# Performance work log

Measured on AMD Instinct MI355X. Metric: run time of the kernel, lower is better.

## Reference

```python
import jax, jax.numpy as jnp
import numpy as np

N = 98304        # total nodes (= 16384 graphs * act_dim 6)
E = 1572864      # edges (avg degree 16)
C = 64           # in_channels
H = 32           # hidden_size
ACT = 6          # act_dim


def setup_inputs() -> dict:
    key = jax.random.key(0)
    ks = jax.random.split(key, 11)
    s = lambda fan: 1.0 / np.sqrt(fan)
    return {
        "state": jax.random.normal(ks[0], (N, C), jnp.float32),
        "edge_index": jax.random.randint(ks[1], (2, E), 0, N, dtype=jnp.int64),
        "conv_W": jax.random.normal(ks[2], (C, C), jnp.float32) * s(C),
        "conv_b": jax.random.normal(ks[3], (C,), jnp.float32) * 0.01,
        "W1": jax.random.normal(ks[4], (C, H), jnp.float32) * s(C),
        "b1": jax.random.normal(ks[5], (H,), jnp.float32) * 0.01,
        "W2": jax.random.normal(ks[6], (H, H), jnp.float32) * s(H),
        "b2": jax.random.normal(ks[7], (H,), jnp.float32) * 0.01,
        "W3": jax.random.normal(ks[8], (H, 1), jnp.float32) * s(H),
        "b3": jax.random.normal(ks[9], (1,), jnp.float32) * 0.01,
    }


def gcn_conv(x, edge_index, W, b):
    # PyG GCNConv: add self-loops, symmetric normalization D^-1/2 (A+I) D^-1/2 (X W) + b
    loops = jnp.arange(N, dtype=edge_index.dtype)
    src = jnp.concatenate([edge_index[0], loops])  # [E+N]
    dst = jnp.concatenate([edge_index[1], loops])  # [E+N]
    deg = jax.ops.segment_sum(jnp.ones(E + N, x.dtype), dst, num_segments=N)
    dinv = jax.lax.rsqrt(deg)                      # deg >= 1 due to self-loops
    norm = dinv[src] * dinv[dst]                   # [E+N]
    h = x @ W                                      # [N, C]
    msg = h[src] * norm[:, None]                   # gather + scale
    return jax.ops.segment_sum(msg, dst, num_segments=N) + b


def reference(state, edge_index, conv_W, conv_b, W1, b1, W2, b2, W3, b3):
    out = jax.nn.relu(gcn_conv(state, edge_index, conv_W, conv_b))
    x = out + state                                # residual
    x = x.reshape(-1, ACT, C)                      # [num_graphs, act_dim, C]
    x = jax.nn.relu(x @ W1 + b1)
    x = jax.nn.relu(x @ W2 + b2)
    x = jax.nn.softplus(x @ W3 + b3)
    concentration = x.squeeze(-1) + 1e-20          # [num_graphs, act_dim]
    return concentration
```

## Files before the change

### kernel.cpp

```cpp
#include <hip/hip_runtime.h>
#include <math.h>

#define Nn 98304
#define Ee 1572864
#define Cc 64
#define Hh 32
#define TT 128
#define NT (Nn / TT)
#define HB 256
#define EPB (Ee / HB)
#define CAPT 2560
#define GN 64


__device__ __forceinline__ int detect64(const void* ei) {
    const unsigned int* u = (const unsigned int*)ei;
    int is64 = 1;
    #pragma unroll
    for (int i = 0; i < 16; ++i) is64 &= (u[2 * i + 1] == 0u);
    return is64;
}

__device__ __forceinline__ int load_idx(const void* ei, long e, int is64) {
    if (is64) return (int)((const long long*)ei)[e];
    return ((const int*)ei)[e];
}

__device__ __forceinline__ unsigned short f2bf(float x) {
    union { float f; unsigned int u; } v; v.f = x;
    unsigned int r = v.u + 0x7FFFu + ((v.u >> 16) & 1u);
    return (unsigned short)(r >> 16);
}
__device__ __forceinline__ float bf2f(unsigned short h) {
    union { unsigned int u; float f; } v; v.u = ((unsigned int)h) << 16;
    return v.f;
}

__device__ __forceinline__ void acc_u4(float a[8], uint4 u) {
    union { unsigned int i; float f; } w;
    w.i = u.x << 16;         a[0] += w.f;
    w.i = u.x & 0xFFFF0000u; a[1] += w.f;
    w.i = u.y << 16;         a[2] += w.f;
    w.i = u.y & 0xFFFF0000u; a[3] += w.f;
    w.i = u.z << 16;         a[4] += w.f;
    w.i = u.z & 0xFFFF0000u; a[5] += w.f;
    w.i = u.w << 16;         a[6] += w.f;
    w.i = u.w & 0xFFFF0000u; a[7] += w.f;
}
__device__ __forceinline__ void set_u4(float a[8], uint4 u) {
    union { unsigned int i; float f; } w;
    w.i = u.x << 16;         a[0] = w.f;
    w.i = u.x & 0xFFFF0000u; a[1] = w.f;
    w.i = u.y << 16;         a[2] = w.f;
    w.i = u.y & 0xFFFF0000u; a[3] = w.f;
    w.i = u.z << 16;         a[4] = w.f;
    w.i = u.z & 0xFFFF0000u; a[5] = w.f;
    w.i = u.w << 16;         a[6] = w.f;
    w.i = u.w & 0xFFFF0000u; a[7] = w.f;
}

__global__ __launch_bounds__(1024) void k_bucket(const void* __restrict__ ei,
                                                 unsigned int* __restrict__ aux,
                                                 unsigned int* __restrict__ ebuf) {
    __shared__ unsigned int hl[NT];
    __shared__ unsigned int off[NT];
    int t = threadIdx.x, b = blockIdx.x;
    if (t < NT) hl[t] = 0;
    __syncthreads();
    int is64 = detect64(ei);
    long e0 = (long)b * EPB;
    #pragma unroll
    for (int i = 0; i < EPB / 1024; ++i) {
        int d = load_idx(ei, (long)Ee + e0 + i * 1024 + t, is64);
        atomicAdd(&hl[d >> 7], 1u);
    }
    __syncthreads();
    if (t < NT) off[t] = hl[t];
    __syncthreads();
    for (int s = 1; s < NT; s <<= 1) {
        unsigned int v = (t < NT && t >= s) ? off[t - s] : 0u;
        __syncthreads();
        if (t < NT) off[t] += v;
        __syncthreads();
    }
    if (t < NT) {
        unsigned int ex = off[t] - hl[t];
        aux[(long)b * NT + t] = ex | (hl[t] << 16);
        off[t] = ex;
    }
    __syncthreads();
    #pragma unroll
    for (int i = 0; i < EPB / 1024; ++i) {
        long e = e0 + i * 1024 + t;
        int s = load_idx(ei, e, is64);
        int d = load_idx(ei, (long)Ee + e, is64);
        unsigned int pos = atomicAdd(&off[d >> 7], 1u);
        ebuf[(long)b * EPB + pos] = (unsigned int)s | ((unsigned int)(d & (TT - 1)) << 17);
    }
}

__global__ __launch_bounds__(256) void k_nodecnt(const unsigned int* __restrict__ aux,
                                                 const unsigned int* __restrict__ ebuf,
                                                 unsigned int* __restrict__ rowOff,
                                                 unsigned int* __restrict__ rowEnd,
                                                 float* __restrict__ dinv,
                                                 unsigned int* __restrict__ srcs) {
    __shared__ unsigned int stage[CAPT];
    __shared__ unsigned int rb[HB];
    __shared__ unsigned int cnt[TT];
    __shared__ unsigned int sc[TT];
    __shared__ unsigned int cur[TT];
    int t = threadIdx.x, tile = blockIdx.x;
    unsigned int av = aux[(long)t * NT + tile];
    unsigned int roff = av & 0xFFFFu, rcnt = av >> 16;
    rb[t] = rcnt;
    __syncthreads();
    for (int s = 1; s < HB; s <<= 1) {
        unsigned int v = (t >= s) ? rb[t - s] : 0u;
        __syncthreads();
        rb[t] += v;
        __syncthreads();
    }
    unsigned int mybase = rb[t] - rcnt;
    for (unsigned int i = 0; i < rcnt; ++i)
        stage[mybase + i] = ebuf[(long)t * EPB + roff + i];
    if (t < TT) cnt[t] = 0;
    __syncthreads();
    int total = (int)rb[HB - 1];
    for (int i = t; i < total; i += 256)
        atomicAdd(&cnt[stage[i] >> 17], 1u);
    __syncthreads();
    if (t < TT) sc[t] = cnt[t];
    __syncthreads();
    #pragma unroll
    for (int off = 1; off < TT; off <<= 1) {
        unsigned int v = (t >= off && t < TT) ? sc[t - off] : 0u;
        __syncthreads();
        if (t < TT) sc[t] += v;
        __syncthreads();
    }
    if (t < TT) {
        unsigned int start = (unsigned int)(tile * CAPT) + sc[t] - cnt[t];
        rowOff[(long)tile * TT + t] = start;
        rowEnd[(long)tile * TT + t] = start + cnt[t];
        cur[t] = start;
        dinv[(long)tile * TT + t] = rsqrtf((float)(cnt[t] + 1));
    }
    __syncthreads();
    for (int i = t; i < total; i += 256) {
        unsigned int u = stage[i];
        unsigned int pos = atomicAdd(&cur[u >> 17], 1u);
        srcs[pos] = u & 0x1FFFFu;
    }
}

__global__ __launch_bounds__(256) void k_gemm(const float* __restrict__ state,
                                              const float* __restrict__ W,
                                              const float* __restrict__ dinv,
                                              unsigned short* __restrict__ gb) {
    __shared__ float Wl[64 * 64];
    __shared__ float Al[64 * 68];
    int t = threadIdx.x;
    long n0 = (long)blockIdx.x * 64;

    const float4* W4 = (const float4*)W;
    float4* Wl4 = (float4*)Wl;
    #pragma unroll
    for (int i = 0; i < 4; ++i) Wl4[i * 256 + t] = W4[i * 256 + t];

    const float4* S4 = (const float4*)(state) + n0 * 16;
    #pragma unroll
    for (int i = 0; i < 4; ++i) {
        int f4 = t + i * 256;
        int r = f4 >> 4, k0 = (f4 & 15) * 4;
        *(float4*)(Al + r * 68 + k0) = S4[f4];
    }
    __syncthreads();

    int r0 = (t >> 4) * 4;
    int c0 = (t & 15) * 4;
    float acc[4][4] = {{0.f}};
    #pragma unroll
    for (int kk = 0; kk < 64; kk += 4) {
        float4 a4[4], w4[4];
        #pragma unroll
        for (int i = 0; i < 4; ++i) a4[i] = *(const float4*)(Al + (r0 + i) * 68 + kk);
        #pragma unroll
        for (int j = 0; j < 4; ++j) w4[j] = *(const float4*)(Wl + (kk + j) * 64 + c0);
        const float* aa = (const float*)a4;
        const float* ww = (const float*)w4;
        #pragma unroll
        for (int i = 0; i < 4; ++i)
            #pragma unroll
            for (int j = 0; j < 4; ++j) {
                float av = aa[i * 4 + j];
                #pragma unroll
                for (int c = 0; c < 4; ++c)
                    acc[i][c] = fmaf(av, ww[j * 4 + c], acc[i][c]);
            }
    }
    #pragma unroll
    for (int i = 0; i < 4; ++i) {
        long n = n0 + r0 + i;
        float dv = dinv[n];
        ushort4 o;
        o.x = f2bf(acc[i][0] * dv); o.y = f2bf(acc[i][1] * dv);
        o.z = f2bf(acc[i][2] * dv); o.w = f2bf(acc[i][3] * dv);
        *(ushort4*)(gb + n * 64 + c0) = o;
    }
}

__global__ __launch_bounds__(512) void k_gf(const unsigned int* __restrict__ rowOff,
                                            const unsigned int* __restrict__ rowEnd,
                                            const unsigned int* __restrict__ srcs,
                                            const unsigned short* __restrict__ gb,
                                            const float* __restrict__ dinv,
                                            const float* __restrict__ state,
                                            const float* __restrict__ conv_b,
                                            const float* __restrict__ W1,
                                            const float* __restrict__ b1,
                                            const float* __restrict__ W2,
                                            const float* __restrict__ b2,
                                            const float* __restrict__ W3,
                                            const float* __restrict__ b3,
                                            float* __restrict__ out) {
    __shared__ float sa[GN * 68];
    __shared__ float hs[GN * 34];
    __shared__ float sW1[Cc * Hh];
    __shared__ float sW2[Hh * Hh];
    __shared__ float sW3[Hh], sb1[Hh], sb2[Hh], scb[Cc];
    __shared__ float sb3;
    int t = threadIdx.x;
    int wave = t >> 6, lane = t & 63;
    long n0 = (long)blockIdx.x * GN;

    for (int i = t; i < Cc * Hh; i += 512) sW1[i] = W1[i];
    for (int i = t; i < Hh * Hh; i += 512) sW2[i] = W2[i];
    if (t < Hh) { sW3[t] = W3[t]; sb1[t] = b1[t]; sb2[t] = b2[t]; }
    if (t >= 64 && t < 128) scb[t - 64] = conv_b[t - 64];
    if (t == 511) sb3 = b3[0];

    {
        int g = lane >> 3;
        int cs = lane & 7;
        int j = wave * 8 + g;
        long n = n0 + j;
        int ptr = (int)rowOff[n];
        int end = (int)rowEnd[n];
        float dv = dinv[n];
        const uint4* gb4 = (const uint4*)gb;

        float a[8];
        set_u4(a, gb4[n * 8 + cs]);

        int cnt = end - ptr;
        while (cnt >= 4) {
            int s0 = (int)srcs[ptr];
            int s1 = (int)srcs[ptr + 1];
            int s2 = (int)srcs[ptr + 2];
            int s3 = (int)srcs[ptr + 3];
            uint4 u0 = gb4[(long)s0 * 8 + cs];
            uint4 u1 = gb4[(long)s1 * 8 + cs];
            uint4 u2 = gb4[(long)s2 * 8 + cs];
            uint4 u3 = gb4[(long)s3 * 8 + cs];
            acc_u4(a, u0); acc_u4(a, u1); acc_u4(a, u2); acc_u4(a, u3);
            ptr += 4; cnt -= 4;
        }
        while (cnt > 0) {
            int s0 = (int)srcs[ptr];
            uint4 u0 = gb4[(long)s0 * 8 + cs];
            acc_u4(a, u0);
            ++ptr; --cnt;
        }

        float* r = sa + j * 68 + cs * 8;
        float4 lo, hi;
        lo.x = a[0] * dv; lo.y = a[1] * dv; lo.z = a[2] * dv; lo.w = a[3] * dv;
        hi.x = a[4] * dv; hi.y = a[5] * dv; hi.z = a[6] * dv; hi.w = a[7] * dv;
        *(float4*)r = lo;
        *(float4*)(r + 4) = hi;
    }
    __syncthreads();

    {
        int j = t >> 3, o = t & 7;
        long n = n0 + j;
        int k0 = o * 8;
        const float4* sp4 = (const float4*)(state + n * 64 + k0);
        float4 s0 = sp4[0], s1 = sp4[1];
        float* r = sa + j * 68 + k0;
        r[0] = fmaxf(r[0] + scb[k0 + 0], 0.f) + s0.x;
        r[1] = fmaxf(r[1] + scb[k0 + 1], 0.f) + s0.y;
        r[2] = fmaxf(r[2] + scb[k0 + 2], 0.f) + s0.z;
        r[3] = fmaxf(r[3] + scb[k0 + 3], 0.f) + s0.w;
        r[4] = fmaxf(r[4] + scb[k0 + 4], 0.f) + s1.x;
        r[5] = fmaxf(r[5] + scb[k0 + 5], 0.f) + s1.y;
        r[6] = fmaxf(r[6] + scb[k0 + 6], 0.f) + s1.z;
        r[7] = fmaxf(r[7] + scb[k0 + 7], 0.f) + s1.w;
    }
    __syncthreads();

    {
        int j = t >> 3, o = t & 7;
        int c0 = o * 4;
        float a0 = sb1[c0], a1 = sb1[c0 + 1], a2 = sb1[c0 + 2], a3 = sb1[c0 + 3];
        #pragma unroll
        for (int k = 0; k < Cc; ++k) {
            float xv = sa[j * 68 + k];
            float4 w = *(const float4*)(sW1 + k * Hh + c0);
            a0 = fmaf(xv, w.x, a0); a1 = fmaf(xv, w.y, a1);
            a2 = fmaf(xv, w.z, a2); a3 = fmaf(xv, w.w, a3);
        }
        float* r = hs + j * 34 + c0;
        r[0] = fmaxf(a0, 0.f); r[1] = fmaxf(a1, 0.f);
        r[2] = fmaxf(a2, 0.f); r[3] = fmaxf(a3, 0.f);
    }
    __syncthreads();

    {
        int j = t >> 3, o = t & 7;
        int c0 = o * 4;
        float a0 = sb2[c0], a1 = sb2[c0 + 1], a2 = sb2[c0 + 2], a3 = sb2[c0 + 3];
        #pragma unroll
        for (int k = 0; k < Hh; ++k) {
            float xv = hs[j * 34 + k];
            float4 w = *(const float4*)(sW2 + k * Hh + c0);
            a0 = fmaf(xv, w.x, a0); a1 = fmaf(xv, w.y, a1);
            a2 = fmaf(xv, w.z, a2); a3 = fmaf(xv, w.w, a3);
        }
        float* r = sa + j * 68 + c0;
        r[0] = fmaxf(a0, 0.f); r[1] = fmaxf(a1, 0.f);
        r[2] = fmaxf(a2, 0.f); r[3] = fmaxf(a3, 0.f);
    }
    __syncthreads();

    if (t < GN) {
        float y = sb3;
        #pragma unroll
        for (int k = 0; k < Hh; ++k) y = fmaf(sa[t * 68 + k], sW3[k], y);
        float sp = fmaxf(y, 0.f) + log1pf(expf(-fabsf(y)));
        out[n0 + t] = sp + 1e-20f;
    }
}

extern "C" void kernel_launch(void* const* d_in, const int* in_sizes, int n_in,
                              void* d_out, int out_size, void* d_ws, size_t ws_size,
                              hipStream_t stream) {
    const float* state  = (const float*)d_in[0];
    const void*  ei     = d_in[1];
    const float* conv_W = (const float*)d_in[2];
    const float* conv_b = (const float*)d_in[3];
    const float* W1 = (const float*)d_in[4];
    const float* b1 = (const float*)d_in[5];
    const float* W2 = (const float*)d_in[6];
    const float* b2 = (const float*)d_in[7];
    const float* W3 = (const float*)d_in[8];
    const float* b3 = (const float*)d_in[9];
    float* out = (float*)d_out;

    float*          dinv   = (float*)d_ws;
    unsigned short* gb     = (unsigned short*)(dinv + Nn);
    unsigned int*   rowOff = (unsigned int*)(gb + (size_t)Nn * 64);
    unsigned int*   rowEnd = rowOff + Nn;
    unsigned int*   aux    = rowEnd + Nn;
    unsigned int*   ebuf   = aux + (size_t)HB * NT;
    unsigned int*   srcs   = ebuf + Ee;

    k_bucket<<<HB, 1024, 0, stream>>>(ei, aux, ebuf);
    k_nodecnt<<<NT, 256, 0, stream>>>(aux, ebuf, rowOff, rowEnd, dinv, srcs);
    k_gemm<<<Nn / 64, 256, 0, stream>>>(state, conv_W, dinv, gb);
    k_gf<<<Nn / GN, 512, 0, stream>>>(rowOff, rowEnd, srcs, gb, dinv, state, conv_b,
                                      W1, b1, W2, b2, W3, b3, out);
}
```

Before: 169.1 us.

## Scatter edges via global per-tile atomics; stage CSR segment in LDS for gather

Replaces the two-pass per-block histogram, scan and scatter bucketing with a single pass that claims positions through global atomic counters, one per 128-node tile and padded to 16 words apart, writing directly into fixed-capacity tile buckets. The tile kernel no longer has to scan and stitch 256 block fragments, which removes the aux table and strided gathers. The gather kernel stages its block's source-index segment in LDS and unrolls the neighbour loop to 8 loads to raise memory-level parallelism. The changes add global atomic contention, make edge order within a tile nondeterministic, and rely on each tile holding no more than CAPT edges, both in the bucket and in the LDS staging buffer.

```diff
diff --git a/kernel.cpp b/kernel.cpp
--- a/kernel.cpp
+++ b/kernel.cpp
@@ -59,74 +59,43 @@
     w.i = u.w & 0xFFFF0000u; a[7] = w.f;
 }
 
-__global__ __launch_bounds__(1024) void k_bucket(const void* __restrict__ ei,
-                                                 unsigned int* __restrict__ aux,
-                                                 unsigned int* __restrict__ ebuf) {
-    __shared__ unsigned int hl[NT];
-    __shared__ unsigned int off[NT];
+__global__ __launch_bounds__(1024) void k_zero(unsigned int* __restrict__ gcur) {
+    gcur[blockIdx.x * 1024 + threadIdx.x] = 0u;
+}
+
+__global__ __launch_bounds__(1024) void k_scat(const void* __restrict__ ei,
+                                               unsigned int* __restrict__ gcur,
+                                               unsigned int* __restrict__ ebuf) {
     int t = threadIdx.x, b = blockIdx.x;
-    if (t < NT) hl[t] = 0;
-    __syncthreads();
     int is64 = detect64(ei);
     long e0 = (long)b * EPB;
-    #pragma unroll
-    for (int i = 0; i < EPB / 1024; ++i) {
-        int d = load_idx(ei, (long)Ee + e0 + i * 1024 + t, is64);
-        atomicAdd(&hl[d >> 7], 1u);
-    }
-    __syncthreads();
-    if (t < NT) off[t] = hl[t];
-    __syncthreads();
-    for (int s = 1; s < NT; s <<= 1) {
-        unsigned int v = (t < NT && t >= s) ? off[t - s] : 0u;
-        __syncthreads();
-        if (t < NT) off[t] += v;
-        __syncthreads();
-    }
-    if (t < NT) {
-        unsigned int ex = off[t] - hl[t];
-        aux[(long)b * NT + t] = ex | (hl[t] << 16);
-        off[t] = ex;
-    }
-    __syncthreads();
     #pragma unroll
     for (int i = 0; i < EPB / 1024; ++i) {
         long e = e0 + i * 1024 + t;
         int s = load_idx(ei, e, is64);
         int d = load_idx(ei, (long)Ee + e, is64);
-        unsigned int pos = atomicAdd(&off[d >> 7], 1u);
-        ebuf[(long)b * EPB + pos] = (unsigned int)s | ((unsigned int)(d & (TT - 1)) << 17);
-    }
-}
-
-__global__ __launch_bounds__(256) void k_nodecnt(const unsigned int* __restrict__ aux,
-                                                 const unsigned int* __restrict__ ebuf,
-                                                 unsigned int* __restrict__ rowOff,
-                                                 unsigned int* __restrict__ rowEnd,
-                                                 float* __restrict__ dinv,
-                                                 unsigned int* __restrict__ srcs) {
+        int tile = d >> 7;
+        unsigned int pos = atomicAdd(&gcur[tile * 16], 1u);
+        ebuf[(long)tile * CAPT + pos] = (unsigned int)s | ((unsigned int)(d & (TT - 1)) << 17);
+    }
+}
+
+__global__ __launch_bounds__(256) void k_tile(const unsigned int* __restrict__ gcur,
+                                              const unsigned int* __restrict__ ebuf,
+                                              unsigned int* __restrict__ rowOff,
+                                              unsigned int* __restrict__ rowEnd,
+                                              float* __restrict__ dinv,
+                                              unsigned int* __restrict__ srcs) {
     __shared__ unsigned int stage[CAPT];
-    __shared__ unsigned int rb[HB];
     __shared__ unsigned int cnt[TT];
     __shared__ unsigned int sc[TT];
     __shared__ unsigned int cur[TT];
     int t = threadIdx.x, tile = blockIdx.x;
-    unsigned int av = aux[(long)t * NT + tile];
-    unsigned int roff = av & 0xFFFFu, rcnt = av >> 16;
-    rb[t] = rcnt;
-    __syncthreads();
-    for (int s = 1; s < HB; s <<= 1) {
-        unsigned int v = (t >= s) ? rb[t - s] : 0u;
-        __syncthreads();
-        rb[t] += v;
-        __syncthreads();
-    }
-    unsigned int mybase = rb[t] - rcnt;
-    for (unsigned int i = 0; i < rcnt; ++i)
-        stage[mybase + i] = ebuf[(long)t * EPB + roff + i];
+    int total = (int)gcur[tile * 16];
     if (t < TT) cnt[t] = 0;
-    __syncthreads();
-    int total = (int)rb[HB - 1];
+    long base = (long)tile * CAPT;
+    for (int i = t; i < total; i += 256) stage[i] = ebuf[base + i];
+    __syncthreads();
     for (int i = t; i < total; i += 256)
         atomicAdd(&cnt[stage[i] >> 17], 1u);
     __syncthreads();
@@ -226,6 +195,7 @@
                                             float* __restrict__ out) {
     __shared__ float sa[GN * 68];
     __shared__ float hs[GN * 34];
+    __shared__ unsigned int sseg[CAPT];
     __shared__ float sW1[Cc * Hh];
     __shared__ float sW2[Hh * Hh];
     __shared__ float sW3[Hh], sb1[Hh], sb2[Hh], scb[Cc];
@@ -240,13 +210,18 @@
     if (t >= 64 && t < 128) scb[t - 64] = conv_b[t - 64];
     if (t == 511) sb3 = b3[0];
 
+    int segBase = (int)rowOff[n0];
+    int segEnd  = (int)rowEnd[n0 + GN - 1];
+    for (int i = segBase + t; i < segEnd; i += 512) sseg[i - segBase] = srcs[i];
+    __syncthreads();
+
     {
         int g = lane >> 3;
         int cs = lane & 7;
         int j = wave * 8 + g;
         long n = n0 + j;
-        int ptr = (int)rowOff[n];
-        int end = (int)rowEnd[n];
+        int ptr = (int)rowOff[n] - segBase;
+        int end = (int)rowEnd[n] - segBase;
         float dv = dinv[n];
         const uint4* gb4 = (const uint4*)gb;
 
@@ -254,11 +229,32 @@
         set_u4(a, gb4[n * 8 + cs]);
 
         int cnt = end - ptr;
-        while (cnt >= 4) {
-            int s0 = (int)srcs[ptr];
-            int s1 = (int)srcs[ptr + 1];
-            int s2 = (int)srcs[ptr + 2];
-            int s3 = (int)srcs[ptr + 3];
+        while (cnt >= 8) {
+            int s0 = (int)sseg[ptr];
+            int s1 = (int)sseg[ptr + 1];
+            int s2 = (int)sseg[ptr + 2];
+            int s3 = (int)sseg[ptr + 3];
+            int s4 = (int)sseg[ptr + 4];
+            int s5 = (int)sseg[ptr + 5];
+            int s6 = (int)sseg[ptr + 6];
+            int s7 = (int)sseg[ptr + 7];
+            uint4 u0 = gb4[(long)s0 * 8 + cs];
+            uint4 u1 = gb4[(long)s1 * 8 + cs];
+            uint4 u2 = gb4[(long)s2 * 8 + cs];
+            uint4 u3 = gb4[(long)s3 * 8 + cs];
+            uint4 u4 = gb4[(long)s4 * 8 + cs];
+            uint4 u5 = gb4[(long)s5 * 8 + cs];
+            uint4 u6 = gb4[(long)s6 * 8 + cs];
+            uint4 u7 = gb4[(long)s7 * 8 + cs];
+            acc_u4(a, u0); acc_u4(a, u1); acc_u4(a, u2); acc_u4(a, u3);
+            acc_u4(a, u4); acc_u4(a, u5); acc_u4(a, u6); acc_u4(a, u7);
+            ptr += 8; cnt -= 8;
+        }
+        if (cnt >= 4) {
+            int s0 = (int)sseg[ptr];
+            int s1 = (int)sseg[ptr + 1];
+            int s2 = (int)sseg[ptr + 2];
+            int s3 = (int)sseg[ptr + 3];
             uint4 u0 = gb4[(long)s0 * 8 + cs];
             uint4 u1 = gb4[(long)s1 * 8 + cs];
             uint4 u2 = gb4[(long)s2 * 8 + cs];
@@ -267,7 +263,7 @@
             ptr += 4; cnt -= 4;
         }
         while (cnt > 0) {
-            int s0 = (int)srcs[ptr];
+            int s0 = (int)sseg[ptr];
             uint4 u0 = gb4[(long)s0 * 8 + cs];
             acc_u4(a, u0);
             ++ptr; --cnt;
@@ -362,12 +358,13 @@
     unsigned short* gb     = (unsigned short*)(dinv + Nn);
     unsigned int*   rowOff = (unsigned int*)(gb + (size_t)Nn * 64);
     unsigned int*   rowEnd = rowOff + Nn;
-    unsigned int*   aux    = rowEnd + Nn;
-    unsigned int*   ebuf   = aux + (size_t)HB * NT;
-    unsigned int*   srcs   = ebuf + Ee;
-
-    k_bucket<<<HB, 1024, 0, stream>>>(ei, aux, ebuf);
-    k_nodecnt<<<NT, 256, 0, stream>>>(aux, ebuf, rowOff, rowEnd, dinv, srcs);
+    unsigned int*   gcur   = rowEnd + Nn;
+    unsigned int*   ebuf   = gcur + (size_t)NT * 16;
+    unsigned int*   srcs   = ebuf + (size_t)NT * CAPT;
+
+    k_zero<<<12, 1024, 0, stream>>>(gcur);
+    k_scat<<<HB, 1024, 0, stream>>>(ei, gcur, ebuf);
+    k_tile<<<NT, 256, 0, stream>>>(gcur, ebuf, rowOff, rowEnd, dinv, srcs);
     k_gemm<<<Nn / 64, 256, 0, stream>>>(state, conv_W, dinv, gb);
     k_gf<<<Nn / GN, 512, 0, stream>>>(rowOff, rowEnd, srcs, gb, dinv, state, conv_b,
                                       W1, b1, W2, b2, W3, b3, out);
```

Result: slower. 244.2 us (+44.5%).
